# Optimization experiments

Hardware: AMD Instinct MI355X
Metric: run time of the kernel (lower is better)

The kernel has to match this reference:

```python
import jax, jax.numpy as jnp
import numpy as np

B, N, D = 4, 512, 128
TAU = 0.5
EPS = 1e-9

def setup_inputs() -> dict:
    key = jax.random.key(0)
    ks = jax.random.split(key, 6)
    sc = 0.05  # weight scale for numerical sanity
    return {
        "entity_states": jax.random.normal(ks[0], (B, N, D), dtype=jnp.float32),
        "Wp": jax.random.normal(ks[1], (D, D), dtype=jnp.float32) * sc,
        "bp": jnp.zeros((D,), dtype=jnp.float32),
        "edge_logits": jax.random.normal(ks[2], (N, N), dtype=jnp.float32),
        "W1": jax.random.normal(ks[3], (2 * D, D), dtype=jnp.float32) * sc,
        "b1": jnp.zeros((D,), dtype=jnp.float32),
        "W2": jax.random.normal(ks[4], (D, D), dtype=jnp.float32) * sc,
        "b2": jnp.zeros((D,), dtype=jnp.float32),
        "u_noise": jax.random.uniform(ks[5], (N, N), dtype=jnp.float32),
    }

def reference(entity_states, Wp, bp, edge_logits, W1, b1, W2, b2, u_noise):
    b, n, d = entity_states.shape
    # entity projection
    proj = entity_states @ Wp + bp  # (B,N,D)
    # gumbel-softmax adjacency (row-wise softmax over sources)
    g = -jnp.log(-jnp.log(u_noise + EPS) + EPS)
    A = jax.nn.softmax((edge_logits + g) / TAU, axis=-1)  # (N,N)
    # split concat-MLP first layer: combined = [source_j, target_i]
    W1_src, W1_tgt = W1[:d], W1[d:]
    s = proj @ W1_src  # (B,N,D) contribution of source j
    t = proj @ W1_tgt  # (B,N,D) contribution of target i
    # h[b,i,j,:] = relu(s[b,j] + t[b,i] + b1)
    h = jax.nn.relu(s[:, None, :, :] + t[:, :, None, :] + b1)  # (B,N,N,D)
    msg = h @ W2 + b2  # (B,N,N,D)
    # weighted aggregation over sources j with A[i,j]
    upd = jnp.einsum('ij,bijd->bid', A, msg)  # (B,N,D)
    next_state = entity_states + upd
    return next_state, jnp.broadcast_to(A, (b, n, n))
```

## Files before the change

kernel.cpp:

```cpp
#include <hip/hip_runtime.h>
#include <math.h>

#define Bv 4
#define Nv 512
#define Dv 128
#define BND (Bv*Nv*Dv)
#define NN  (Nv*Nv)
#define EPSv 1e-9f

typedef float f2 __attribute__((ext_vector_type(2)));

__global__ __launch_bounds__(256) void k_prep(
    const float* __restrict__ ES, const float* __restrict__ Wp,
    const float* __restrict__ bp, const float* __restrict__ W1,
    const float* __restrict__ b1, const float* __restrict__ EL,
    const float* __restrict__ UN,
    float* __restrict__ s_out, float* __restrict__ t_out,
    float* __restrict__ A_out)
{
    __shared__ float es[4][Dv];
    __shared__ float pr[4][Dv];
    __shared__ float sred[4];
    const int bi = blockIdx.x;
    const int t  = threadIdx.x;

    {
        const int row = bi;
        const float u0 = UN[row*Nv + t];
        const float u1 = UN[row*Nv + t + 256];
        const float g0 = -logf(-logf(u0 + EPSv) + EPSv);
        const float g1 = -logf(-logf(u1 + EPSv) + EPSv);
        const float z0 = (EL[row*Nv + t]       + g0) * 2.0f;
        const float z1 = (EL[row*Nv + t + 256] + g1) * 2.0f;

        float m = fmaxf(z0, z1);
        #pragma unroll
        for (int off = 32; off >= 1; off >>= 1)
            m = fmaxf(m, __shfl_xor(m, off, 64));
        if ((t & 63) == 0) sred[t >> 6] = m;
        __syncthreads();
        m = fmaxf(fmaxf(sred[0], sred[1]), fmaxf(sred[2], sred[3]));

        const float e0 = expf(z0 - m);
        const float e1 = expf(z1 - m);
        float ssum = e0 + e1;
        #pragma unroll
        for (int off = 32; off >= 1; off >>= 1)
            ssum += __shfl_xor(ssum, off, 64);
        __syncthreads();
        if ((t & 63) == 0) sred[t >> 6] = ssum;
        __syncthreads();
        const float inv = 1.0f / (sred[0] + sred[1] + sred[2] + sred[3]);
        const float a0 = e0 * inv;
        const float a1 = e1 * inv;
        #pragma unroll
        for (int bb = 0; bb < Bv; ++bb) {
            A_out[bb*NN + row*Nv + t]       = a0;
            A_out[bb*NN + row*Nv + t + 256] = a1;
        }
    }

    const int row0 = bi * 4;
    const int c  = t & 127;
    const int rg = t >> 7;

    for (int idx = t; idx < 4*Dv; idx += 256)
        es[idx >> 7][idx & 127] = ES[(row0 + (idx >> 7))*Dv + (idx & 127)];
    __syncthreads();

    {
        float acc[2];
        const float bpc = bp[c];
        acc[0] = bpc; acc[1] = bpc;
        #pragma unroll 8
        for (int k = 0; k < Dv; ++k) {
            const float w = Wp[k*Dv + c];
            acc[0] = fmaf(es[rg*2][k],   w, acc[0]);
            acc[1] = fmaf(es[rg*2+1][k], w, acc[1]);
        }
        pr[rg*2][c]   = acc[0];
        pr[rg*2+1][c] = acc[1];
    }
    __syncthreads();

    float sacc0 = b1[c], sacc1 = sacc0, tacc0 = 0.0f, tacc1 = 0.0f;
    #pragma unroll 8
    for (int k = 0; k < Dv; ++k) {
        const float ws_ = W1[k*Dv + c];
        const float wt_ = W1[(Dv + k)*Dv + c];
        const float p0 = pr[rg*2][k];
        const float p1 = pr[rg*2+1][k];
        sacc0 = fmaf(p0, ws_, sacc0);
        sacc1 = fmaf(p1, ws_, sacc1);
        tacc0 = fmaf(p0, wt_, tacc0);
        tacc1 = fmaf(p1, wt_, tacc1);
    }
    const int ra = (row0 + rg*2)*Dv + c;
    s_out[ra]      = sacc0;
    s_out[ra + Dv] = sacc1;
    t_out[ra]      = tacc0;
    t_out[ra + Dv] = tacc1;
}

__global__ __launch_bounds__(256) void k_main(
    const float* __restrict__ s_buf, const float* __restrict__ t_buf,
    const float* __restrict__ A0,    const float* __restrict__ ES,
    const float* __restrict__ W2,    const float* __restrict__ b2,
    float* __restrict__ out)
{
    const int JT = 128;
    __shared__ float sj[JT][Dv];
    const int i0 = blockIdx.x * 4;
    const int b  = blockIdx.y;
    const int t  = threadIdx.x;
    const int d  = t & 127;
    const int p  = __builtin_amdgcn_readfirstlane(t >> 7);
    const int ia = i0 + 2*p;

    f2 tv;
    tv.x = t_buf[(b*Nv + ia)*Dv + d];
    tv.y = t_buf[(b*Nv + ia + 1)*Dv + d];
    const float* __restrict__ Ar0 = A0 + ia*Nv;
    const float* __restrict__ Ar1 = A0 + (ia + 1)*Nv;

    f2 acc; acc.x = 0.0f; acc.y = 0.0f;
    for (int jt = 0; jt < Nv; jt += JT) {
        __syncthreads();
        const float4* __restrict__ src = (const float4*)(s_buf + (b*Nv + jt)*Dv);
        float4* dst = (float4*)(&sj[0][0]);
        #pragma unroll
        for (int u = 0; u < 16; ++u)
            dst[t + u*256] = src[t + u*256];
        __syncthreads();
        #pragma unroll 4
        for (int j = 0; j < JT; ++j) {
            const float a0 = Ar0[jt + j];
            const float a1 = Ar1[jt + j];
            const float sv = sj[j][d];
            f2 z; z.x = sv + tv.x; z.y = sv + tv.y;
            f2 r; r.x = fmaxf(z.x, 0.0f); r.y = fmaxf(z.y, 0.0f);
            acc.x = fmaf(a0, r.x, acc.x);
            acc.y = fmaf(a1, r.y, acc.y);
        }
    }

    __syncthreads();
    sj[2*p][d]     = acc.x;
    sj[2*p + 1][d] = acc.y;
    __syncthreads();

    const int c  = t & 127;
    const int rg = t >> 7;
    float o0 = b2[c], o1 = o0;
    #pragma unroll 8
    for (int k = 0; k < Dv; ++k) {
        const float w2 = W2[k*Dv + c];
        o0 = fmaf(sj[rg*2][k],   w2, o0);
        o1 = fmaf(sj[rg*2+1][k], w2, o1);
    }
    const int ro0 = (b*Nv + i0 + rg*2)*Dv + c;
    out[ro0]      = ES[ro0]      + o0;
    out[ro0 + Dv] = ES[ro0 + Dv] + o1;
}

extern "C" void kernel_launch(void* const* d_in, const int* in_sizes, int n_in,
                              void* d_out, int out_size, void* d_ws, size_t ws_size,
                              hipStream_t stream) {
    (void)in_sizes; (void)n_in; (void)out_size; (void)ws_size;
    const float* ES = (const float*)d_in[0];
    const float* Wp = (const float*)d_in[1];
    const float* bp = (const float*)d_in[2];
    const float* EL = (const float*)d_in[3];
    const float* W1 = (const float*)d_in[4];
    const float* b1 = (const float*)d_in[5];
    const float* W2 = (const float*)d_in[6];
    const float* b2 = (const float*)d_in[7];
    const float* UN = (const float*)d_in[8];

    float* out   = (float*)d_out;
    float* A_out = out + BND;

    float* s_buf = (float*)d_ws;
    float* t_buf = s_buf + BND;

    k_prep<<<512, 256, 0, stream>>>(ES, Wp, bp, W1, b1, EL, UN,
                                    s_buf, t_buf, A_out);
    k_main<<<dim3(Nv/4, Bv), 256, 0, stream>>>(s_buf, t_buf, A_out, ES, W2, b2,
                                               out);
}
```

Measured before the change: 114.0 us.

## Register-tile k_main over 8 target rows and 4 dims with split-j reduction

Restructures the main aggregation kernel so each block handles 8 target rows. Each thread keeps an 8x4 register tile of accumulators and reads s rows straight from global memory as float4. The block's A rows are staged in LDS, and the source dimension j is split across 8 thread groups whose partial sums are reduced through shared memory before the W2 projection. This raises arithmetic intensity per s load and removes the per-tile s staging and barriers. In exchange it halves the grid to 256 blocks and adds register pressure and an LDS reduction step.

Measured after the change: 110.2 us. -3.3%, faster.

```diff
diff --git a/kernel.cpp b/kernel.cpp
--- a/kernel.cpp
+++ b/kernel.cpp
@@ -8,7 +8,17 @@
 #define NN  (Nv*Nv)
 #define EPSv 1e-9f
 
-typedef float f2 __attribute__((ext_vector_type(2)));
+typedef float f4 __attribute__((ext_vector_type(4)));
+
+__device__ __forceinline__ f4 relu4(f4 z) {
+#if __has_builtin(__builtin_elementwise_max)
+    return __builtin_elementwise_max(z, (f4)0.0f);
+#else
+    z.x = fmaxf(z.x, 0.0f); z.y = fmaxf(z.y, 0.0f);
+    z.z = fmaxf(z.z, 0.0f); z.w = fmaxf(z.w, 0.0f);
+    return z;
+#endif
+}
 
 __global__ __launch_bounds__(256) void k_prep(
     const float* __restrict__ ES, const float* __restrict__ Wp,
@@ -108,59 +118,91 @@
     const float* __restrict__ W2,    const float* __restrict__ b2,
     float* __restrict__ out)
 {
-    const int JT = 128;
-    __shared__ float sj[JT][Dv];
-    const int i0 = blockIdx.x * 4;
+    __shared__ float A_lds[8][Nv];
+    __shared__ f4    part[8][8][32];
+    __shared__ float hsum[8][Dv];
+    const int i0 = blockIdx.x * 8;
     const int b  = blockIdx.y;
     const int t  = threadIdx.x;
-    const int d  = t & 127;
-    const int p  = __builtin_amdgcn_readfirstlane(t >> 7);
-    const int ia = i0 + 2*p;
-
-    f2 tv;
-    tv.x = t_buf[(b*Nv + ia)*Dv + d];
-    tv.y = t_buf[(b*Nv + ia + 1)*Dv + d];
-    const float* __restrict__ Ar0 = A0 + ia*Nv;
-    const float* __restrict__ Ar1 = A0 + (ia + 1)*Nv;
-
-    f2 acc; acc.x = 0.0f; acc.y = 0.0f;
-    for (int jt = 0; jt < Nv; jt += JT) {
-        __syncthreads();
-        const float4* __restrict__ src = (const float4*)(s_buf + (b*Nv + jt)*Dv);
-        float4* dst = (float4*)(&sj[0][0]);
-        #pragma unroll
-        for (int u = 0; u < 16; ++u)
+    const int dq = t & 31;
+    const int jg = t >> 5;
+
+    {
+        const f4* __restrict__ src = (const f4*)(A0 + i0*Nv);
+        f4* dst = (f4*)(&A_lds[0][0]);
+        #pragma unroll
+        for (int u = 0; u < 4; ++u)
             dst[t + u*256] = src[t + u*256];
-        __syncthreads();
-        #pragma unroll 4
-        for (int j = 0; j < JT; ++j) {
-            const float a0 = Ar0[jt + j];
-            const float a1 = Ar1[jt + j];
-            const float sv = sj[j][d];
-            f2 z; z.x = sv + tv.x; z.y = sv + tv.y;
-            f2 r; r.x = fmaxf(z.x, 0.0f); r.y = fmaxf(z.y, 0.0f);
-            acc.x = fmaf(a0, r.x, acc.x);
-            acc.y = fmaf(a1, r.y, acc.y);
-        }
-    }
-
-    __syncthreads();
-    sj[2*p][d]     = acc.x;
-    sj[2*p + 1][d] = acc.y;
-    __syncthreads();
-
-    const int c  = t & 127;
-    const int rg = t >> 7;
-    float o0 = b2[c], o1 = o0;
-    #pragma unroll 8
-    for (int k = 0; k < Dv; ++k) {
-        const float w2 = W2[k*Dv + c];
-        o0 = fmaf(sj[rg*2][k],   w2, o0);
-        o1 = fmaf(sj[rg*2+1][k], w2, o1);
-    }
-    const int ro0 = (b*Nv + i0 + rg*2)*Dv + c;
-    out[ro0]      = ES[ro0]      + o0;
-    out[ro0 + Dv] = ES[ro0 + Dv] + o1;
+    }
+
+    f4 tv[8];
+    #pragma unroll
+    for (int r = 0; r < 8; ++r)
+        tv[r] = *(const f4*)(t_buf + (b*Nv + i0 + r)*Dv + dq*4);
+
+    f4 acc[8];
+    #pragma unroll
+    for (int r = 0; r < 8; ++r) acc[r] = (f4)0.0f;
+
+    __syncthreads();
+
+    const float* __restrict__ sb = s_buf + (size_t)b*Nv*Dv + dq*4;
+    const int j0 = jg*64;
+    for (int j4 = j0; j4 < j0 + 64; j4 += 4) {
+        f4 a[8];
+        #pragma unroll
+        for (int r = 0; r < 8; ++r)
+            a[r] = *(const f4*)(&A_lds[r][j4]);
+        #pragma unroll
+        for (int u = 0; u < 4; ++u) {
+            const f4 sv = *(const f4*)(sb + (j4 + u)*Dv);
+            #pragma unroll
+            for (int r = 0; r < 8; ++r) {
+                f4 z = relu4(sv + tv[r]);
+                acc[r] += a[r][u] * z;
+            }
+        }
+    }
+
+    #pragma unroll
+    for (int r = 0; r < 8; ++r) part[jg][r][dq] = acc[r];
+    __syncthreads();
+    {
+        const int ri = t >> 5;
+        f4 s = part[0][ri][dq];
+        #pragma unroll
+        for (int g = 1; g < 8; ++g) s += part[g][ri][dq];
+        *(f4*)(&hsum[ri][dq*4]) = s;
+    }
+    __syncthreads();
+
+    const int cg = t & 63;
+    const int rg = t >> 6;
+    const int c0 = 2*cg;
+    const int r0 = 2*rg;
+    float o00 = b2[c0], o01 = b2[c0+1];
+    float o10 = o00,    o11 = o01;
+    for (int k4 = 0; k4 < Dv; k4 += 4) {
+        const f4 h0 = *(const f4*)(&hsum[r0][k4]);
+        const f4 h1 = *(const f4*)(&hsum[r0+1][k4]);
+        #pragma unroll
+        for (int u = 0; u < 4; ++u) {
+            const float2 w = *(const float2*)(W2 + (k4 + u)*Dv + c0);
+            o00 = fmaf(h0[u], w.x, o00);
+            o01 = fmaf(h0[u], w.y, o01);
+            o10 = fmaf(h1[u], w.x, o10);
+            o11 = fmaf(h1[u], w.y, o11);
+        }
+    }
+    const int ro0 = (b*Nv + i0 + r0)*Dv + c0;
+    const int ro1 = ro0 + Dv;
+    const float2 e0 = *(const float2*)(ES + ro0);
+    const float2 e1 = *(const float2*)(ES + ro1);
+    float2 v0, v1;
+    v0.x = e0.x + o00; v0.y = e0.y + o01;
+    v1.x = e1.x + o10; v1.y = e1.y + o11;
+    *(float2*)(out + ro0) = v0;
+    *(float2*)(out + ro1) = v1;
 }
 
 extern "C" void kernel_launch(void* const* d_in, const int* in_sizes, int n_in,
@@ -185,6 +227,6 @@
 
     k_prep<<<512, 256, 0, stream>>>(ES, Wp, bp, W1, b1, EL, UN,
                                     s_buf, t_buf, A_out);
-    k_main<<<dim3(Nv/4, Bv), 256, 0, stream>>>(s_buf, t_buf, A_out, ES, W2, b2,
+    k_main<<<dim3(Nv/8, Bv), 256, 0, stream>>>(s_buf, t_buf, A_out, ES, W2, b2,
                                                out);
 }
```
